# Kernel tuning notes

Hardware: AMD Instinct MI355X
Metric: run time of the kernel (lower is better)

Reference implementation:

```python
import jax, jax.numpy as jnp
import numpy as np

EPS = 1e-10


def setup_inputs() -> dict:
    key = jax.random.key(0)
    k1, k2 = jax.random.split(key)
    B, N = 4096, 10000
    pred = jax.random.uniform(k1, (B, N), dtype=jnp.float32)
    y = jax.random.randint(k2, (B, N), 0, 2, dtype=jnp.int32)
    return {"pred": pred, "y": y, "lamda": 5}


def reference(pred, y, lamda):
    # per-element weighted BCE-style term:
    #   y==0 -> -log(1 - p + eps); y!=0 -> -lamda * log(p + eps)
    neg_term = -jnp.log1p(-(pred - EPS))          # -log(1 - p + eps)
    pos_term = -lamda * jnp.log(pred + EPS)
    elem = jnp.where(y == 0, neg_term, pos_term)  # [B, N]
    # mean over elements per sample, then mean over batch; keep shape (1,) like torch.zeros(1)
    loss = jnp.mean(elem)
    return loss.reshape(1)
```

## Files before the change

kernel.cpp:

```cpp
#include <hip/hip_runtime.h>
#include <hip/hip_bf16.h>

#define EPS 1e-10f
#define GRID1 2048
#define BLOCK 256


__global__ __launch_bounds__(BLOCK) void sparse_loss_stage1(
    const float* __restrict__ pred,
    const int* __restrict__ y,
    const int* __restrict__ lamda_p,
    float* __restrict__ partials,
    long long nvec,
    long long total) {
  const float lam = (float)(*lamda_p);

  float acc = 0.0f;

  const long long tid = (long long)blockIdx.x * blockDim.x + threadIdx.x;
  const long long stride = (long long)gridDim.x * blockDim.x;

  const float4* __restrict__ pv = reinterpret_cast<const float4*>(pred);
  const int4* __restrict__ yv = reinterpret_cast<const int4*>(y);

  long long i = tid;

#define ELEM(P, Y)                                              \
  {                                                             \
    const bool z = ((Y) == 0);                                  \
    const float a = EPS + (z ? (1.0f - (P)) : (P));             \
    const float c = z ? 1.0f : lam;                             \
    acc = fmaf(c, __logf(a), acc);                              \
  }
#define VEC4(P, Y)                                              \
  ELEM(P.x, Y.x) ELEM(P.y, Y.y) ELEM(P.z, Y.z) ELEM(P.w, Y.w)

  for (; i + 3 * stride < nvec; i += 4 * stride) {
    float4 p0 = pv[i];
    float4 p1 = pv[i + stride];
    float4 p2 = pv[i + 2 * stride];
    float4 p3 = pv[i + 3 * stride];
    int4 y0 = yv[i];
    int4 y1 = yv[i + stride];
    int4 y2 = yv[i + 2 * stride];
    int4 y3 = yv[i + 3 * stride];
    VEC4(p0, y0)
    VEC4(p1, y1)
    VEC4(p2, y2)
    VEC4(p3, y3)
  }

  for (; i < nvec; i += stride) {
    float4 p = pv[i];
    int4 yy = yv[i];
    VEC4(p, yy)
  }

  for (long long j = nvec * 4 + tid; j < total; j += stride) {
    const float p = pred[j];
    ELEM(p, y[j])
  }
#undef VEC4
#undef ELEM

  for (int off = 32; off > 0; off >>= 1)
    acc += __shfl_down(acc, off, 64);

  __shared__ float ssum[4];
  const int lane = threadIdx.x & 63;
  const int wave = threadIdx.x >> 6;
  if (lane == 0) ssum[wave] = acc;
  __syncthreads();

  if (threadIdx.x == 0)
    partials[blockIdx.x] = ssum[0] + ssum[1] + ssum[2] + ssum[3];
}

__global__ __launch_bounds__(BLOCK) void sparse_loss_stage2(
    const float* __restrict__ partials,
    float* __restrict__ out,
    float inv_total) {
  float acc = 0.0f;
  for (int i = threadIdx.x; i < GRID1; i += BLOCK)
    acc += partials[i];

  for (int off = 32; off > 0; off >>= 1)
    acc += __shfl_down(acc, off, 64);

  __shared__ float ssum[4];
  const int lane = threadIdx.x & 63;
  const int wave = threadIdx.x >> 6;
  if (lane == 0) ssum[wave] = acc;
  __syncthreads();

  if (threadIdx.x == 0) {
    out[0] = -(ssum[0] + ssum[1] + ssum[2] + ssum[3]) * inv_total;
  }
}

extern "C" void kernel_launch(void* const* d_in, const int* in_sizes, int n_in,
                              void* d_out, int out_size, void* d_ws, size_t ws_size,
                              hipStream_t stream) {
  const float* pred = (const float*)d_in[0];
  const int* y = (const int*)d_in[1];
  const int* lamda = (const int*)d_in[2];
  float* out = (float*)d_out;
  float* partials = (float*)d_ws;

  const long long total = (long long)in_sizes[0];
  const long long nvec = total / 4;
  const float inv_total = 1.0f / (float)total;

  sparse_loss_stage1<<<GRID1, BLOCK, 0, stream>>>(pred, y, lamda, partials,
                                                  nvec, total);
  sparse_loss_stage2<<<1, BLOCK, 0, stream>>>(partials, out, inv_total);
}
```

Measured before the change: 333.9 us.

## Switch stage-1 to block-contiguous tiles with 8 vector loads in flight per thread

Replaces the grid-strided loop, which kept four float4/int4 pairs in flight, with per-block contiguous tiles of 2048 vectors. Each thread issues 8 float4 and 8 int4 loads before computing. The aim is more memory-level parallelism and better DRAM locality per block on a bandwidth-bound streaming reduction. The cost is higher register pressure, and the tile count (about 5000 tiles over 2048 blocks) leaves the blocks unevenly loaded.

New measurement: 330.1 us. No clear change (-1.1%).

```diff
diff --git a/kernel.cpp b/kernel.cpp
--- a/kernel.cpp
+++ b/kernel.cpp
@@ -2,8 +2,9 @@
 #include <hip/hip_bf16.h>
 
 #define EPS 1e-10f
+#define BLOCK 256
 #define GRID1 2048
-#define BLOCK 256
+#define TILE_VEC (BLOCK * 8)
 
 
 __global__ __launch_bounds__(BLOCK) void sparse_loss_stage1(
@@ -14,16 +15,13 @@
     long long nvec,
     long long total) {
   const float lam = (float)(*lamda_p);
-
   float acc = 0.0f;
-
-  const long long tid = (long long)blockIdx.x * blockDim.x + threadIdx.x;
-  const long long stride = (long long)gridDim.x * blockDim.x;
 
   const float4* __restrict__ pv = reinterpret_cast<const float4*>(pred);
   const int4* __restrict__ yv = reinterpret_cast<const int4*>(y);
 
-  long long i = tid;
+  const long long ntiles = (nvec + TILE_VEC - 1) / TILE_VEC;
+  const int tid = threadIdx.x;
 
 #define ELEM(P, Y)                                              \
   {                                                             \
@@ -32,47 +30,57 @@
     const float c = z ? 1.0f : lam;                             \
     acc = fmaf(c, __logf(a), acc);                              \
   }
-#define VEC4(P, Y)                                              \
-  ELEM(P.x, Y.x) ELEM(P.y, Y.y) ELEM(P.z, Y.z) ELEM(P.w, Y.w)
 
-  for (; i + 3 * stride < nvec; i += 4 * stride) {
-    float4 p0 = pv[i];
-    float4 p1 = pv[i + stride];
-    float4 p2 = pv[i + 2 * stride];
-    float4 p3 = pv[i + 3 * stride];
-    int4 y0 = yv[i];
-    int4 y1 = yv[i + stride];
-    int4 y2 = yv[i + 2 * stride];
-    int4 y3 = yv[i + 3 * stride];
-    VEC4(p0, y0)
-    VEC4(p1, y1)
-    VEC4(p2, y2)
-    VEC4(p3, y3)
+  for (long long tile = blockIdx.x; tile < ntiles; tile += gridDim.x) {
+    const long long base = tile * TILE_VEC;
+    const float4* __restrict__ pt = pv + base;
+    const int4* __restrict__ yt = yv + base;
+    const long long rem = nvec - base;
+
+    if (rem >= TILE_VEC) {
+      float4 p[8];
+      int4 yy[8];
+#pragma unroll
+      for (int k = 0; k < 8; ++k) p[k] = pt[tid + BLOCK * k];
+#pragma unroll
+      for (int k = 0; k < 8; ++k) yy[k] = yt[tid + BLOCK * k];
+#pragma unroll
+      for (int k = 0; k < 8; ++k) {
+        ELEM(p[k].x, yy[k].x)
+        ELEM(p[k].y, yy[k].y)
+        ELEM(p[k].z, yy[k].z)
+        ELEM(p[k].w, yy[k].w)
+      }
+    } else {
+      for (long long j = tid; j < rem; j += BLOCK) {
+        const float4 p = pt[j];
+        const int4 yy = yt[j];
+        ELEM(p.x, yy.x)
+        ELEM(p.y, yy.y)
+        ELEM(p.z, yy.z)
+        ELEM(p.w, yy.w)
+      }
+    }
   }
 
-  for (; i < nvec; i += stride) {
-    float4 p = pv[i];
-    int4 yy = yv[i];
-    VEC4(p, yy)
-  }
-
-  for (long long j = nvec * 4 + tid; j < total; j += stride) {
+  const long long gtid = (long long)blockIdx.x * BLOCK + tid;
+  const long long gstride = (long long)gridDim.x * BLOCK;
+  for (long long j = nvec * 4 + gtid; j < total; j += gstride) {
     const float p = pred[j];
     ELEM(p, y[j])
   }
-#undef VEC4
 #undef ELEM
 
   for (int off = 32; off > 0; off >>= 1)
     acc += __shfl_down(acc, off, 64);
 
   __shared__ float ssum[4];
-  const int lane = threadIdx.x & 63;
-  const int wave = threadIdx.x >> 6;
+  const int lane = tid & 63;
+  const int wave = tid >> 6;
   if (lane == 0) ssum[wave] = acc;
   __syncthreads();
 
-  if (threadIdx.x == 0)
+  if (tid == 0)
     partials[blockIdx.x] = ssum[0] + ssum[1] + ssum[2] + ssum[3];
 }
 
@@ -93,9 +101,8 @@
   if (lane == 0) ssum[wave] = acc;
   __syncthreads();
 
-  if (threadIdx.x == 0) {
+  if (threadIdx.x == 0)
     out[0] = -(ssum[0] + ssum[1] + ssum[2] + ssum[3]) * inv_total;
-  }
 }
 
 extern "C" void kernel_launch(void* const* d_in, const int* in_sizes, int n_in,
```
